# Optimization experiments

Measured on AMD Instinct MI355X. Metric: run time of the kernel, lower is better.

Reference implementation:

```python
import jax, jax.numpy as jnp
import numpy as np

N, E, F_NODE, F_EDGE, H = 50000, 800000, 64, 32, 64
NT, ET, ETE = 3, 4, 4  # num node types, num edge types, edge-type embedding dim
NEG = 0.2              # leaky_relu negative slope (PyG HEATConv default)


def hetero_lin(x, t, W, b):
    # per-type linear: x [N,in], t [N] int, W [T,in,out], b [T,out]
    outs = jnp.einsum('ni,tio->tno', x, W) + b[:, None, :]   # [T,N,out]
    return outs[t, jnp.arange(x.shape[0])]                   # [N,out]


def segment_softmax(logits, seg, num_segments):
    m = jax.ops.segment_max(logits, seg, num_segments=num_segments)
    ex = jnp.exp(logits - m[seg])
    s = jax.ops.segment_sum(ex, seg, num_segments=num_segments)
    return ex / (s[seg] + 1e-16)


def eheat_conv(x, src, dst, node_type, edge_type, edge_attr, Whl, bhl, Ete, Wea, Watt, Wlin):
    n = x.shape[0]
    h = hetero_lin(x, node_type, Whl, bhl)            # [N,H]
    ete = jax.nn.leaky_relu(Ete[edge_type], NEG)      # [E,ETE]
    ea = jax.nn.leaky_relu(edge_attr @ Wea, NEG)      # [E,H] edge embedding (returned)
    xi, xj = h[dst], h[src]                           # gather target/source node feats
    # attention logits = leaky_relu(att(cat([x_i, x_j, ete, ea]))); Watt split to avoid big concat
    Wi, Wj, Wt, We = Watt[:H], Watt[H:2 * H], Watt[2 * H:2 * H + ETE], Watt[2 * H + ETE:]
    logits = jax.nn.leaky_relu(xi @ Wi + xj @ Wj + ete @ Wt + ea @ We, NEG)[:, 0]  # [E]
    alpha = segment_softmax(logits, dst, n)           # softmax over incoming edges of dst
    # message = lin(cat([x_j, ea])) * alpha ; scatter-add at dst (heads=1, dropout eval=identity)
    msg = (xj @ Wlin[:H] + ea @ Wlin[H:]) * alpha[:, None]   # [E,H]
    out = jax.ops.segment_sum(msg, dst, num_segments=n)     # [N,H]
    return out, ea


def setup_inputs():
    key = jax.random.key(0)
    ks = jax.random.split(key, 40)
    def rnd(i, shape):
        return jax.random.normal(ks[i], shape, dtype=jnp.float32) * 0.1
    inp = {
        'x': jax.random.normal(ks[0], (N, F_NODE), dtype=jnp.float32),
        'edge_index': jax.random.randint(ks[1], (2, E), 0, N),
        'node_type': jax.random.randint(ks[2], (N,), 0, NT),
        'edge_type': jax.random.randint(ks[3], (E,), 0, ET),
        'edge_attr': jax.random.normal(ks[4], (E, F_EDGE), dtype=jnp.float32),
    }
    node_ins = [F_NODE, H, H]
    edge_ins = [F_EDGE, H, H]
    i = 5
    for l in range(3):
        inp[f'Whl{l+1}'] = rnd(i, (NT, node_ins[l], H)); i += 1
        inp[f'bhl{l+1}'] = jnp.zeros((NT, H), jnp.float32)
        inp[f'Ete{l+1}'] = rnd(i, (ET, ETE)); i += 1
        inp[f'Wea{l+1}'] = rnd(i, (edge_ins[l], H)); i += 1
        inp[f'Watt{l+1}'] = rnd(i, (2 * H + ETE + H, 1)); i += 1
        inp[f'Wlin{l+1}'] = rnd(i, (2 * H, H)); i += 1
    inp['Wnc'] = rnd(i, (NT, H, 1)); i += 1
    inp['bnc'] = jnp.zeros((NT, 1), jnp.float32)
    inp['Wec'] = rnd(i, (ET, H, 1)); i += 1
    inp['bec'] = jnp.zeros((ET, 1), jnp.float32)
    return inp


def reference(x, edge_index, node_type, edge_type, edge_attr,
              Whl1, bhl1, Ete1, Wea1, Watt1, Wlin1,
              Whl2, bhl2, Ete2, Wea2, Watt2, Wlin2,
              Whl3, bhl3, Ete3, Wea3, Watt3, Wlin3,
              Wnc, bnc, Wec, bec):
    src, dst = edge_index[0], edge_index[1]
    h, e = eheat_conv(x, src, dst, node_type, edge_type, edge_attr,
                      Whl1, bhl1, Ete1, Wea1, Watt1, Wlin1)
    h, e = jax.nn.relu(h), jax.nn.relu(e)   # dropout is identity in eval mode
    h, e = eheat_conv(h, src, dst, node_type, edge_type, e,
                      Whl2, bhl2, Ete2, Wea2, Watt2, Wlin2)
    h, e = jax.nn.relu(h), jax.nn.relu(e)
    h, e = eheat_conv(h, src, dst, node_type, edge_type, e,
                      Whl3, bhl3, Ete3, Wea3, Watt3, Wlin3)
    h, e = jax.nn.relu(h), jax.nn.relu(e)
    x_out = hetero_lin(h, node_type, Wnc, bnc)   # [N,1]
    e_out = hetero_lin(e, edge_type, Wec, bec)   # [E,1]
    return (x_out, e_out)
```

## Files before the change

### kernel.cpp

```cpp
#include <hip/hip_runtime.h>
#include <hip/hip_bf16.h>

#define NEG 0.2f
#define LRELU(x) ((x) > 0.f ? (x) : NEG*(x))

typedef __hip_bfloat16 bf16;
typedef __attribute__((ext_vector_type(8))) short short8v;
typedef __attribute__((ext_vector_type(4))) float f32x4;

__device__ __forceinline__ float b2f(bf16 v){ return __bfloat162float(v); }
__device__ __forceinline__ float ldf(const float* p, size_t i){ return p[i]; }
__device__ __forceinline__ float ldf(const bf16* p, size_t i){ return __bfloat162float(p[i]); }

__device__ __forceinline__ float wred(float v){
#pragma unroll
  for(int o=32;o>0;o>>=1) v += __shfl_down(v,o);
  return v;
}

__device__ __forceinline__ float atomAddF(float* p, float v){
  return __hip_atomic_fetch_add(p, v, __ATOMIC_RELAXED, __HIP_MEMORY_SCOPE_AGENT);
}
__device__ __forceinline__ int atomAddI(int* p, int v){
  return __hip_atomic_fetch_add(p, v, __ATOMIC_RELAXED, __HIP_MEMORY_SCOPE_AGENT);
}


__global__ __launch_bounds__(256) void k_hist(
    const int* __restrict__ dst, int* __restrict__ deg, int nE)
{
  int e = blockIdx.x*blockDim.x + threadIdx.x;
  if (e >= nE) return;
  atomAddI(&deg[dst[e]], 1);
}

__global__ __launch_bounds__(1024) void k_scan(
    const int* __restrict__ deg, int* __restrict__ off, int nN)
{
  __shared__ int part[1024];
  int tid = threadIdx.x;
  int chunk = (nN + 1023) / 1024;
  int lo = tid*chunk, hi = min((tid+1)*chunk, nN);
  int s = 0;
  for (int i=lo;i<hi;i++) s += deg[i];
  part[tid] = s;
  __syncthreads();
  for (int d=1; d<1024; d<<=1){
    int v = (tid>=d) ? part[tid-d] : 0;
    __syncthreads();
    part[tid] += v;
    __syncthreads();
  }
  int run = (tid==0) ? 0 : part[tid-1];
  for (int i=lo;i<hi;i++){ off[i] = run; run += deg[i]; }
  if (tid==1023) off[nN] = part[1023];
}

__global__ __launch_bounds__(256) void k_scatter(
    const int* __restrict__ dst, const int* __restrict__ off,
    int* __restrict__ cnt, int* __restrict__ eid, int nE)
{
  int e = blockIdx.x*blockDim.x + threadIdx.x;
  if (e >= nE) return;
  int d = dst[e];
  int p = atomAddI(&cnt[d], 1);
  eid[off[d] + p] = e;
}


template<typename TIN, bool RELU_IN>
__global__ __launch_bounds__(256) void k_hlin(
    const TIN* __restrict__ xin, const int* __restrict__ ntype,
    const float* __restrict__ Whl, const float* __restrict__ bhl,
    const float* __restrict__ Watt,
    bf16* __restrict__ h, float* __restrict__ hi_s, float* __restrict__ hj_s,
    int nN)
{
  int wid  = (blockIdx.x*blockDim.x + threadIdx.x) >> 6;
  int lane = threadIdx.x & 63;
  if (wid >= nN) return;
  int t = ntype[wid];
  float xv = ldf(xin, (size_t)wid*64 + lane);
  if (RELU_IN) xv = fmaxf(xv, 0.f);
  const float* W = Whl + (size_t)t*4096;
  float acc = bhl[t*64 + lane];
#pragma unroll
  for (int i=0;i<64;i++) acc = fmaf(__shfl(xv, i), W[i*64 + lane], acc);
  h[(size_t)wid*64 + lane] = __float2bfloat16(acc);
  float pi = wred(acc * Watt[lane]);
  float pj = wred(acc * Watt[64 + lane]);
  if (lane==0){ hi_s[wid]=pi; hj_s[wid]=pj; }
}

__global__ __launch_bounds__(256) void k_bfrag(
    const float* __restrict__ W, bf16* __restrict__ frag, int KS)
{
  int t = blockIdx.x*blockDim.x + threadIdx.x;
  int total = 4*KS*64;
  if (t >= total) return;
  int lane = t & 63;
  int ks = (t>>6) % KS;
  int nt = (t>>6) / KS;
  int kb = lane>>4, col = lane&15;
#pragma unroll
  for (int j=0;j<8;j++){
    frag[((size_t)(nt*KS+ks)*64 + lane)*8 + j] =
      __float2bfloat16(W[(ks*32 + kb*8 + j)*64 + nt*16 + col]);
  }
}

template<int LAYER>
__global__ __launch_bounds__(256) void k_ea_mfma(
    const void* __restrict__ ain_, const bf16* __restrict__ bfrag,
    const float* __restrict__ Watt,
    const int* __restrict__ src, const int* __restrict__ dst,
    const int* __restrict__ etype, const float* __restrict__ Ete,
    const float* __restrict__ hi_s, const float* __restrict__ hj_s,
    bf16* __restrict__ eout, float* __restrict__ exbuf, float* __restrict__ segsum,
    const float* __restrict__ Wec, const float* __restrict__ bec,
    float* __restrict__ e_out, int nE)
{
  constexpr int KS = (LAYER==0) ? 1 : 2;
  int wid  = (blockIdx.x*blockDim.x + threadIdx.x) >> 6;
  int lane = threadIdx.x & 63;
  int e0 = wid * 16;
  if (e0 >= nE) return;
  int row = lane & 15;
  int kb  = lane >> 4;
  int er  = min(e0 + row, nE-1);

  short8v a[KS];
  if (LAYER==0) {
    const float* A = (const float*)ain_;
    const float* p = A + (size_t)er*32 + kb*8;
#pragma unroll
    for (int j=0;j<8;j++){
      bf16 b = __float2bfloat16(p[j]);
      a[0][j] = *reinterpret_cast<short*>(&b);
    }
  } else {
    const bf16* A = (const bf16*)ain_;
#pragma unroll
    for (int ks=0; ks<KS; ks++){
      short8v v = *reinterpret_cast<const short8v*>(
          reinterpret_cast<const short*>(A + (size_t)er*64 + ks*32 + kb*8));
#pragma unroll
      for (int j=0;j<8;j++) v[j] = (v[j] & (short)0x8000) ? (short)0 : v[j];
      a[ks] = v;
    }
  }

  f32x4 acc[4];
#pragma unroll
  for (int nt=0; nt<4; nt++){
    f32x4 c = {0.f,0.f,0.f,0.f};
#pragma unroll
    for (int ks=0; ks<KS; ks++){
      short8v b = *reinterpret_cast<const short8v*>(
          reinterpret_cast<const short*>(bfrag) + (((size_t)nt*KS + ks)*64 + lane)*8);
      c = __builtin_amdgcn_mfma_f32_16x16x32_bf16(a[ks], b, c, 0, 0, 0);
    }
#pragma unroll
    for (int r=0;r<4;r++) c[r] = LRELU(c[r]);
    acc[nt] = c;
  }

#pragma unroll
  for (int r=0;r<4;r++){
    int e = e0 + kb*4 + r;
    if (e < nE){
#pragma unroll
      for (int nt=0;nt<4;nt++)
        eout[(size_t)e*64 + nt*16 + row] = __float2bfloat16(acc[nt][r]);
    }
  }

#pragma unroll
  for (int r=0;r<4;r++){
    int e = e0 + kb*4 + r;
    bool valid = (e < nE);
    int t = valid ? etype[e] : 0;
    float lp = 0.f, pe = 0.f;
#pragma unroll
    for (int nt=0;nt<4;nt++) lp = fmaf(acc[nt][r], Watt[132 + nt*16 + row], lp);
    if (LAYER==2){
#pragma unroll
      for (int nt=0;nt<4;nt++) pe = fmaf(fmaxf(acc[nt][r],0.f), Wec[t*64 + nt*16 + row], pe);
    }
#pragma unroll
    for (int m=1;m<16;m<<=1){
      lp += __shfl_xor(lp, m);
      if (LAYER==2) pe += __shfl_xor(pe, m);
    }
    if (row == 0 && valid){
      int d = dst[e], s = src[e];
      float wt = 0.f;
#pragma unroll
      for (int k=0;k<4;k++){ float v = Ete[t*4+k]; v = LRELU(v); wt = fmaf(v, Watt[128+k], wt); }
      float l = lp + hi_s[d] + hj_s[s] + wt;
      l = LRELU(l);
      float ex = __expf(fminf(l, 60.f));
      exbuf[e] = ex;
      atomAddF(&segsum[d], ex);
      if (LAYER==2) e_out[e] = pe + bec[t];
    }
  }
}

__global__ __launch_bounds__(256) void k_inv(float* __restrict__ segsum, int nN)
{
  int n = blockIdx.x*blockDim.x + threadIdx.x;
  if (n >= nN) return;
  segsum[n] = 1.f / (segsum[n] + 1e-16f);
}

__global__ __launch_bounds__(256) void k_agg(
    const int* __restrict__ off, const int* __restrict__ eid,
    const int* __restrict__ src,
    const bf16* __restrict__ h, const bf16* __restrict__ ea,
    const float* __restrict__ ex, const float* __restrict__ inv_segsum,
    bf16* __restrict__ uv, int nN)
{
  int wid  = (blockIdx.x*blockDim.x + threadIdx.x) >> 6;
  int lane = threadIdx.x & 63;
  if (wid >= nN) return;
  int beg = off[wid], end = off[wid+1];
  float inv = inv_segsum[wid];
  float au = 0.f, av = 0.f;
  int i = beg;
  int eC = 0, sC = 0; float aC = 0.f;
  if (i < end){ eC = eid[i]; sC = src[eC]; aC = ex[eC]; }
  while (i < end){
    int e = eC, s = sC; float a = aC * inv;
    int j = i + 1;
    if (j < end){ eC = eid[j]; sC = src[eC]; aC = ex[eC]; }
    float hv = b2f(h[(size_t)s*64 + lane]);
    float ev = b2f(ea[(size_t)e*64 + lane]);
    au = fmaf(a, hv, au);
    av = fmaf(a, ev, av);
    i = j;
  }
  uv[(size_t)wid*128 + lane]      = __float2bfloat16(au);
  uv[(size_t)wid*128 + 64 + lane] = __float2bfloat16(av);
}

__global__ __launch_bounds__(256) void k_mm_mfma(
    const bf16* __restrict__ uv, const bf16* __restrict__ bfrag,
    float* __restrict__ out, int nN)
{
  int wid  = (blockIdx.x*blockDim.x + threadIdx.x) >> 6;
  int lane = threadIdx.x & 63;
  int n0 = wid * 16;
  if (n0 >= nN) return;
  int row = lane & 15;
  int kb  = lane >> 4;
  int nr  = min(n0 + row, nN-1);

  short8v a[4];
#pragma unroll
  for (int ks=0; ks<4; ks++)
    a[ks] = *reinterpret_cast<const short8v*>(
        reinterpret_cast<const short*>(uv + (size_t)nr*128 + ks*32 + kb*8));

  f32x4 acc[4];
#pragma unroll
  for (int nt=0; nt<4; nt++){
    f32x4 c = {0.f,0.f,0.f,0.f};
#pragma unroll
    for (int ks=0; ks<4; ks++){
      short8v b = *reinterpret_cast<const short8v*>(
          reinterpret_cast<const short*>(bfrag) + (((size_t)nt*4 + ks)*64 + lane)*8);
      c = __builtin_amdgcn_mfma_f32_16x16x32_bf16(a[ks], b, c, 0, 0, 0);
    }
    acc[nt] = c;
  }

#pragma unroll
  for (int r=0;r<4;r++){
    int n = n0 + kb*4 + r;
    if (n < nN){
#pragma unroll
      for (int nt=0;nt<4;nt++)
        out[(size_t)n*64 + nt*16 + row] = acc[nt][r];
    }
  }
}

__global__ __launch_bounds__(256) void k_xout(
    const float* __restrict__ hin, const int* __restrict__ ntype,
    const float* __restrict__ Wnc, const float* __restrict__ bnc,
    float* __restrict__ xout, int nN)
{
  int wid  = (blockIdx.x*blockDim.x + threadIdx.x) >> 6;
  int lane = threadIdx.x & 63;
  if (wid >= nN) return;
  int t = ntype[wid];
  float v = fmaxf(hin[(size_t)wid*64 + lane], 0.f);
  float p = wred(v * Wnc[t*64 + lane]);
  if (lane==0) xout[wid] = p + bnc[t];
}

extern "C" void kernel_launch(void* const* d_in, const int* in_sizes, int n_in,
                              void* d_out, int out_size, void* d_ws, size_t ws_size,
                              hipStream_t stream) {
  const float* x      = (const float*)d_in[0];
  const int*   eidx   = (const int*) d_in[1];
  const int*   ntype  = (const int*) d_in[2];
  const int*   etype  = (const int*) d_in[3];
  const float* eattr  = (const float*)d_in[4];
  const float* Whl[3]  = {(const float*)d_in[5],  (const float*)d_in[11], (const float*)d_in[17]};
  const float* bhl[3]  = {(const float*)d_in[6],  (const float*)d_in[12], (const float*)d_in[18]};
  const float* Ete[3]  = {(const float*)d_in[7],  (const float*)d_in[13], (const float*)d_in[19]};
  const float* Wea[3]  = {(const float*)d_in[8],  (const float*)d_in[14], (const float*)d_in[20]};
  const float* Watt[3] = {(const float*)d_in[9],  (const float*)d_in[15], (const float*)d_in[21]};
  const float* Wlin[3] = {(const float*)d_in[10], (const float*)d_in[16], (const float*)d_in[22]};
  const float* Wnc = (const float*)d_in[23];
  const float* bnc = (const float*)d_in[24];
  const float* Wec = (const float*)d_in[25];
  const float* bec = (const float*)d_in[26];

  const int nN = in_sizes[2];
  const int nE = in_sizes[3];
  const int* srcI = eidx;
  const int* dstI = eidx + nE;

  float* ws = (float*)d_ws;
  size_t o = 0;
  bf16*  h      = (bf16*)(ws + o); o += (size_t)nN*32;
  float* outA   = ws + o;
  bf16*  uv     = (bf16*)(ws + o); o += (size_t)nN*64;
  float* hi_s   = ws + o;          o += (size_t)nN;
  float* hj_s   = ws + o;          o += (size_t)nN;
  float* exbuf  = ws + o;          o += (size_t)nE;
  float* segsum = ws + o;          o += (size_t)nN;
  bf16*  ea     = (bf16*)(ws + o); o += (size_t)nE*32;
  int*   deg    = (int*)(ws + o);  o += (size_t)nN;
  int*   off    = (int*)(ws + o);  o += (size_t)nN + 1;
  int*   eid    = (int*)(ws + o);  o += (size_t)nE;
  o = (o + 3) & ~(size_t)3;
  bf16*  bfrag  = (bf16*)(ws + o); o += (size_t)4096;

  dim3 blk(256);
  int nodeWB = (int)(((size_t)nN*64 + 255)/256);
  int edgeTB = (nE + 255)/256;
  int nodeTB = (nN + 255)/256;
  int eaMB   = (int)(((size_t)((nE+15)/16)*64 + 255)/256);
  int mmMB   = (int)(((size_t)((nN+15)/16)*64 + 255)/256);

  hipMemsetAsync(deg, 0, (size_t)nN*4, stream);
  k_hist<<<edgeTB, blk, 0, stream>>>(dstI, deg, nE);
  k_scan<<<1, 1024, 0, stream>>>(deg, off, nN);
  hipMemsetAsync(deg, 0, (size_t)nN*4, stream);
  k_scatter<<<edgeTB, blk, 0, stream>>>(dstI, off, deg, eid, nE);

  float* xout = (float*)d_out;

  for (int L = 0; L < 3; ++L) {
    if (L == 0)
      k_hlin<float,false><<<nodeWB, blk, 0, stream>>>(x,    ntype, Whl[L], bhl[L], Watt[L], h, hi_s, hj_s, nN);
    else
      k_hlin<float,true ><<<nodeWB, blk, 0, stream>>>(outA, ntype, Whl[L], bhl[L], Watt[L], h, hi_s, hj_s, nN);

    hipMemsetAsync(segsum, 0, (size_t)nN*4, stream);

    int KS = (L==0) ? 1 : 2;
    k_bfrag<<<(4*KS*64 + 255)/256, blk, 0, stream>>>(Wea[L], bfrag, KS);
    if (L == 0)
      k_ea_mfma<0><<<eaMB, blk, 0, stream>>>(eattr, bfrag, Watt[L], srcI, dstI, etype, Ete[L],
                                             hi_s, hj_s, ea, exbuf, segsum, nullptr, nullptr, nullptr, nE);
    else if (L == 1)
      k_ea_mfma<1><<<eaMB, blk, 0, stream>>>(ea, bfrag, Watt[L], srcI, dstI, etype, Ete[L],
                                             hi_s, hj_s, ea, exbuf, segsum, nullptr, nullptr, nullptr, nE);
    else
      k_ea_mfma<2><<<eaMB, blk, 0, stream>>>(ea, bfrag, Watt[L], srcI, dstI, etype, Ete[L],
                                             hi_s, hj_s, ea, exbuf, segsum, Wec, bec, xout + nN, nE);

    k_inv<<<nodeTB, blk, 0, stream>>>(segsum, nN);
    k_agg<<<nodeWB, blk, 0, stream>>>(off, eid, srcI, h, ea, exbuf, segsum, uv, nN);

    k_bfrag<<<(4*4*64 + 255)/256, blk, 0, stream>>>(Wlin[L], bfrag, 4);
    k_mm_mfma<<<mmMB, blk, 0, stream>>>(uv, bfrag, outA, nN);
  }

  k_xout<<<nodeWB, blk, 0, stream>>>(outA, ntype, Wnc, bnc, xout, nN);
}
```

Before: 1.053 ms.

## Store edges in destination-sorted order and fold softmax normalization into aggregation

A one-time permutation kernel builds dst-sorted copies of src, dst and edge type. All edge-level buffers (edge embeddings, exp logits) are then kept in that sorted order, so the aggregation reads them contiguously instead of through eid indirection. Segment sums are accumulated inside the aggregation loop, which removes the float atomics, the per-layer memset and the inverse kernel. The cost is a gathered read of the layer-0 edge_attr and a scattered write of e_out through eid, plus extra workspace for the permuted index arrays.

Result: faster. 928.6 us (-11.8%).

```diff
diff --git a/kernel.cpp b/kernel.cpp
--- a/kernel.cpp
+++ b/kernel.cpp
@@ -18,9 +18,6 @@
   return v;
 }
 
-__device__ __forceinline__ float atomAddF(float* p, float v){
-  return __hip_atomic_fetch_add(p, v, __ATOMIC_RELAXED, __HIP_MEMORY_SCOPE_AGENT);
-}
 __device__ __forceinline__ int atomAddI(int* p, int v){
   return __hip_atomic_fetch_add(p, v, __ATOMIC_RELAXED, __HIP_MEMORY_SCOPE_AGENT);
 }
@@ -67,6 +64,19 @@
   eid[off[d] + p] = e;
 }
 
+__global__ __launch_bounds__(256) void k_perm(
+    const int* __restrict__ eid, const int* __restrict__ src,
+    const int* __restrict__ dst, const int* __restrict__ ety,
+    int* __restrict__ srcP, int* __restrict__ dstP, int* __restrict__ etyP, int nE)
+{
+  int i = blockIdx.x*blockDim.x + threadIdx.x;
+  if (i >= nE) return;
+  int e = eid[i];
+  srcP[i] = src[e];
+  dstP[i] = dst[e];
+  etyP[i] = ety[e];
+}
+
 
 template<typename TIN, bool RELU_IN>
 __global__ __launch_bounds__(256) void k_hlin(
@@ -111,12 +121,12 @@
 
 template<int LAYER>
 __global__ __launch_bounds__(256) void k_ea_mfma(
-    const void* __restrict__ ain_, const bf16* __restrict__ bfrag,
-    const float* __restrict__ Watt,
-    const int* __restrict__ src, const int* __restrict__ dst,
-    const int* __restrict__ etype, const float* __restrict__ Ete,
+    const void* __restrict__ ain_, const int* __restrict__ eid,
+    const bf16* __restrict__ bfrag, const float* __restrict__ Watt,
+    const int* __restrict__ srcP, const int* __restrict__ dstP,
+    const int* __restrict__ etyP, const float* __restrict__ Ete,
     const float* __restrict__ hi_s, const float* __restrict__ hj_s,
-    bf16* __restrict__ eout, float* __restrict__ exbuf, float* __restrict__ segsum,
+    bf16* __restrict__ eaS, float* __restrict__ exS,
     const float* __restrict__ Wec, const float* __restrict__ bec,
     float* __restrict__ e_out, int nE)
 {
@@ -132,7 +142,7 @@
   short8v a[KS];
   if (LAYER==0) {
     const float* A = (const float*)ain_;
-    const float* p = A + (size_t)er*32 + kb*8;
+    const float* p = A + (size_t)eid[er]*32 + kb*8;
 #pragma unroll
     for (int j=0;j<8;j++){
       bf16 b = __float2bfloat16(p[j]);
@@ -171,7 +181,7 @@
     if (e < nE){
 #pragma unroll
       for (int nt=0;nt<4;nt++)
-        eout[(size_t)e*64 + nt*16 + row] = __float2bfloat16(acc[nt][r]);
+        eaS[(size_t)e*64 + nt*16 + row] = __float2bfloat16(acc[nt][r]);
     }
   }
 
@@ -179,7 +189,7 @@
   for (int r=0;r<4;r++){
     int e = e0 + kb*4 + r;
     bool valid = (e < nE);
-    int t = valid ? etype[e] : 0;
+    int t = valid ? etyP[e] : 0;
     float lp = 0.f, pe = 0.f;
 #pragma unroll
     for (int nt=0;nt<4;nt++) lp = fmaf(acc[nt][r], Watt[132 + nt*16 + row], lp);
@@ -193,55 +203,46 @@
       if (LAYER==2) pe += __shfl_xor(pe, m);
     }
     if (row == 0 && valid){
-      int d = dst[e], s = src[e];
+      int d = dstP[e], s = srcP[e];
       float wt = 0.f;
 #pragma unroll
       for (int k=0;k<4;k++){ float v = Ete[t*4+k]; v = LRELU(v); wt = fmaf(v, Watt[128+k], wt); }
       float l = lp + hi_s[d] + hj_s[s] + wt;
       l = LRELU(l);
-      float ex = __expf(fminf(l, 60.f));
-      exbuf[e] = ex;
-      atomAddF(&segsum[d], ex);
-      if (LAYER==2) e_out[e] = pe + bec[t];
-    }
-  }
-}
-
-__global__ __launch_bounds__(256) void k_inv(float* __restrict__ segsum, int nN)
-{
-  int n = blockIdx.x*blockDim.x + threadIdx.x;
-  if (n >= nN) return;
-  segsum[n] = 1.f / (segsum[n] + 1e-16f);
+      exS[e] = __expf(fminf(l, 60.f));
+      if (LAYER==2) e_out[eid[e]] = pe + bec[t];
+    }
+  }
 }
 
 __global__ __launch_bounds__(256) void k_agg(
-    const int* __restrict__ off, const int* __restrict__ eid,
-    const int* __restrict__ src,
-    const bf16* __restrict__ h, const bf16* __restrict__ ea,
-    const float* __restrict__ ex, const float* __restrict__ inv_segsum,
+    const int* __restrict__ off, const int* __restrict__ srcP,
+    const bf16* __restrict__ h, const bf16* __restrict__ eaS,
+    const float* __restrict__ exS,
     bf16* __restrict__ uv, int nN)
 {
   int wid  = (blockIdx.x*blockDim.x + threadIdx.x) >> 6;
   int lane = threadIdx.x & 63;
   if (wid >= nN) return;
   int beg = off[wid], end = off[wid+1];
-  float inv = inv_segsum[wid];
-  float au = 0.f, av = 0.f;
+  float au = 0.f, av = 0.f, ss = 0.f;
   int i = beg;
-  int eC = 0, sC = 0; float aC = 0.f;
-  if (i < end){ eC = eid[i]; sC = src[eC]; aC = ex[eC]; }
+  int sC = 0; float aC = 0.f;
+  if (i < end){ sC = srcP[i]; aC = exS[i]; }
   while (i < end){
-    int e = eC, s = sC; float a = aC * inv;
+    int s = sC; float a = aC;
     int j = i + 1;
-    if (j < end){ eC = eid[j]; sC = src[eC]; aC = ex[eC]; }
+    if (j < end){ sC = srcP[j]; aC = exS[j]; }
     float hv = b2f(h[(size_t)s*64 + lane]);
-    float ev = b2f(ea[(size_t)e*64 + lane]);
+    float ev = b2f(eaS[(size_t)i*64 + lane]);
     au = fmaf(a, hv, au);
     av = fmaf(a, ev, av);
+    ss += a;
     i = j;
   }
-  uv[(size_t)wid*128 + lane]      = __float2bfloat16(au);
-  uv[(size_t)wid*128 + 64 + lane] = __float2bfloat16(av);
+  float inv = 1.f / (ss + 1e-16f);
+  uv[(size_t)wid*128 + lane]      = __float2bfloat16(au * inv);
+  uv[(size_t)wid*128 + 64 + lane] = __float2bfloat16(av * inv);
 }
 
 __global__ __launch_bounds__(256) void k_mm_mfma(
@@ -331,19 +332,20 @@
   bf16*  uv     = (bf16*)(ws + o); o += (size_t)nN*64;
   float* hi_s   = ws + o;          o += (size_t)nN;
   float* hj_s   = ws + o;          o += (size_t)nN;
-  float* exbuf  = ws + o;          o += (size_t)nE;
-  float* segsum = ws + o;          o += (size_t)nN;
-  bf16*  ea     = (bf16*)(ws + o); o += (size_t)nE*32;
+  float* exS    = ws + o;          o += (size_t)nE;
+  bf16*  eaS    = (bf16*)(ws + o); o += (size_t)nE*32;
   int*   deg    = (int*)(ws + o);  o += (size_t)nN;
   int*   off    = (int*)(ws + o);  o += (size_t)nN + 1;
   int*   eid    = (int*)(ws + o);  o += (size_t)nE;
+  int*   srcP   = (int*)(ws + o);  o += (size_t)nE;
+  int*   dstP   = (int*)(ws + o);  o += (size_t)nE;
+  int*   etyP   = (int*)(ws + o);  o += (size_t)nE;
   o = (o + 3) & ~(size_t)3;
   bf16*  bfrag  = (bf16*)(ws + o); o += (size_t)4096;
 
   dim3 blk(256);
   int nodeWB = (int)(((size_t)nN*64 + 255)/256);
   int edgeTB = (nE + 255)/256;
-  int nodeTB = (nN + 255)/256;
   int eaMB   = (int)(((size_t)((nE+15)/16)*64 + 255)/256);
   int mmMB   = (int)(((size_t)((nN+15)/16)*64 + 255)/256);
 
@@ -352,6 +354,7 @@
   k_scan<<<1, 1024, 0, stream>>>(deg, off, nN);
   hipMemsetAsync(deg, 0, (size_t)nN*4, stream);
   k_scatter<<<edgeTB, blk, 0, stream>>>(dstI, off, deg, eid, nE);
+  k_perm<<<edgeTB, blk, 0, stream>>>(eid, srcI, dstI, etype, srcP, dstP, etyP, nE);
 
   float* xout = (float*)d_out;
 
@@ -361,22 +364,19 @@
     else
       k_hlin<float,true ><<<nodeWB, blk, 0, stream>>>(outA, ntype, Whl[L], bhl[L], Watt[L], h, hi_s, hj_s, nN);
 
-    hipMemsetAsync(segsum, 0, (size_t)nN*4, stream);
-
     int KS = (L==0) ? 1 : 2;
     k_bfrag<<<(4*KS*64 + 255)/256, blk, 0, stream>>>(Wea[L], bfrag, KS);
     if (L == 0)
-      k_ea_mfma<0><<<eaMB, blk, 0, stream>>>(eattr, bfrag, Watt[L], srcI, dstI, etype, Ete[L],
-                                             hi_s, hj_s, ea, exbuf, segsum, nullptr, nullptr, nullptr, nE);
+      k_ea_mfma<0><<<eaMB, blk, 0, stream>>>(eattr, eid, bfrag, Watt[L], srcP, dstP, etyP, Ete[L],
+                                             hi_s, hj_s, eaS, exS, nullptr, nullptr, nullptr, nE);
     else if (L == 1)
-      k_ea_mfma<1><<<eaMB, blk, 0, stream>>>(ea, bfrag, Watt[L], srcI, dstI, etype, Ete[L],
-                                             hi_s, hj_s, ea, exbuf, segsum, nullptr, nullptr, nullptr, nE);
+      k_ea_mfma<1><<<eaMB, blk, 0, stream>>>(eaS, eid, bfrag, Watt[L], srcP, dstP, etyP, Ete[L],
+                                             hi_s, hj_s, eaS, exS, nullptr, nullptr, nullptr, nE);
     else
-      k_ea_mfma<2><<<eaMB, blk, 0, stream>>>(ea, bfrag, Watt[L], srcI, dstI, etype, Ete[L],
-                                             hi_s, hj_s, ea, exbuf, segsum, Wec, bec, xout + nN, nE);
-
-    k_inv<<<nodeTB, blk, 0, stream>>>(segsum, nN);
-    k_agg<<<nodeWB, blk, 0, stream>>>(off, eid, srcI, h, ea, exbuf, segsum, uv, nN);
+      k_ea_mfma<2><<<eaMB, blk, 0, stream>>>(eaS, eid, bfrag, Watt[L], srcP, dstP, etyP, Ete[L],
+                                             hi_s, hj_s, eaS, exS, Wec, bec, xout + nN, nE);
+
+    k_agg<<<nodeWB, blk, 0, stream>>>(off, srcP, h, eaS, exS, uv, nN);
 
     k_bfrag<<<(4*4*64 + 255)/256, blk, 0, stream>>>(Wlin[L], bfrag, 4);
     k_mm_mfma<<<mmMB, blk, 0, stream>>>(uv, bfrag, outA, nN);
```
